# Kernel optimization log

Measured on AMD Instinct MI355X. Metric: run time of the kernel, lower is better.

## Reference

```python
import jax, jax.numpy as jnp
import numpy as np

B, S, DM, H = 4, 2048, 1024, 16
D = DM // H  # head dim = 64

def setup_inputs() -> dict:
    key = jax.random.key(0)
    ks = jax.random.split(key, 7)
    s = 0.02
    return {
        "hidden_states": jax.random.normal(ks[0], (B, S, DM), jnp.float32),
        "attention_mask": jnp.zeros((B, 1, 1, S), jnp.float32),
        "Wq": jax.random.normal(ks[1], (DM, DM), jnp.float32) * s,
        "bq": jnp.zeros((DM,), jnp.float32),
        "Wk": jax.random.normal(ks[2], (DM, DM), jnp.float32) * s,
        "bk": jnp.zeros((DM,), jnp.float32),
        "Wv": jax.random.normal(ks[3], (DM, DM), jnp.float32) * s,
        "bv": jnp.zeros((DM,), jnp.float32),
    }

def _heads(x):
    # [B,S,DM] -> [B,H,S,D]
    return x.reshape(B, S, H, D).transpose(0, 2, 1, 3)

def reference(hidden_states, attention_mask, Wq, bq, Wk, bk, Wv, bv):
    q = _heads(hidden_states @ Wq + bq)
    k = _heads(hidden_states @ Wk + bk)
    v = _heads(hidden_states @ Wv + bv)
    scores = jnp.einsum("bhqd,bhkd->bhqk", q, k) / jnp.sqrt(jnp.float32(D))
    scores = scores + attention_mask
    probs = jax.nn.softmax(scores, axis=-1)  # dropout p=0 -> identity
    ctx = jnp.einsum("bhqk,bhkd->bhqd", probs, v)
    ctx = ctx.transpose(0, 2, 1, 3).reshape(B, S, DM)
    return (ctx, probs)
```

## Files before the change

### kernel.cpp

```cpp
#include <hip/hip_runtime.h>

#define SEQ    2048
#define DMODEL 1024
#define NHEAD  16
#define HDIM   64
#define NBATCH 4
#define LOG2E  1.44269504088896f

typedef __bf16 bf16x8 __attribute__((ext_vector_type(8)));
typedef float  f32x4  __attribute__((ext_vector_type(4)));
typedef unsigned short ushort8_t __attribute__((ext_vector_type(8)));
typedef unsigned short ushort4_t __attribute__((ext_vector_type(4)));

__device__ __forceinline__ unsigned short bfc(float f) {
  union { __bf16 h; unsigned short u; } v;
  v.h = (__bf16)f;
  return v.u;
}

__device__ __forceinline__ float fexp2(float x) {
#if __has_builtin(__builtin_amdgcn_exp2f)
  return __builtin_amdgcn_exp2f(x);
#else
  return exp2f(x);
#endif
}

__device__ __forceinline__ void glds16(const void* g, void* l) {
  __builtin_amdgcn_global_load_lds(
      (const __attribute__((address_space(1))) unsigned int*)g,
      (__attribute__((address_space(3))) unsigned int*)l, 16, 0, 0);
}

__global__ __launch_bounds__(256) void xconv(
    const float* __restrict__ X, unsigned short* __restrict__ Xb)
{
  const size_t i = ((size_t)blockIdx.x * 256 + threadIdx.x) * 8;
  const float4 f0 = *reinterpret_cast<const float4*>(X + i);
  const float4 f1 = *reinterpret_cast<const float4*>(X + i + 4);
  ushort8_t u;
  u[0]=bfc(f0.x); u[1]=bfc(f0.y); u[2]=bfc(f0.z); u[3]=bfc(f0.w);
  u[4]=bfc(f1.x); u[5]=bfc(f1.y); u[6]=bfc(f1.z); u[7]=bfc(f1.w);
  *reinterpret_cast<ushort8_t*>(Xb + i) = u;
}

__global__ __launch_bounds__(256) void wt_kernel(
    const float* __restrict__ W0, const float* __restrict__ W1,
    const float* __restrict__ W2, unsigned short* __restrict__ Wt)
{
  const int k0 = blockIdx.x * 64;
  const int n0 = blockIdx.y * 64;
  const int w  = blockIdx.z;
  const float* W = (w == 0) ? W0 : (w == 1) ? W1 : W2;
  const float scale = (w == 0) ? 0.125f * LOG2E : 1.0f;
  unsigned short* dst = Wt + (size_t)w * DMODEL * DMODEL;

  __shared__ __align__(16) unsigned short T[64][72];
  const int t = threadIdx.x;

  #pragma unroll
  for (int i = 0; i < 4; ++i) {
    const int slot = t + i * 256;
    const int row  = slot >> 4;
    const int c4   = (slot & 15) * 4;
    const float4 f = *reinterpret_cast<const float4*>(W + (size_t)(k0 + row) * DMODEL + n0 + c4);
    ushort4_t u;
    u.x = bfc(f.x * scale); u.y = bfc(f.y * scale);
    u.z = bfc(f.z * scale); u.w = bfc(f.w * scale);
    *reinterpret_cast<ushort4_t*>(&T[row][c4]) = u;
  }
  __syncthreads();
  #pragma unroll
  for (int i = 0; i < 2; ++i) {
    const int slot = t + i * 256;
    const int n  = slot >> 3;
    const int k8 = (slot & 7) * 8;
    ushort8_t v;
    #pragma unroll
    for (int j = 0; j < 8; ++j) v[j] = T[k8 + j][n];
    *reinterpret_cast<ushort8_t*>(dst + (size_t)(n0 + n) * DMODEL + k0 + k8) = v;
  }
}

__global__ __launch_bounds__(256) void qkv_gemm(
    const unsigned short* __restrict__ Xb, const unsigned short* __restrict__ Wt,
    const float* __restrict__ bq, const float* __restrict__ bk, const float* __restrict__ bv,
    unsigned short* __restrict__ Qh, unsigned short* __restrict__ Kh, unsigned short* __restrict__ Vh)
{
  const int m0  = blockIdx.x * 128;
  const int n0g = blockIdx.y * 128;
  const int w   = n0g >> 10;
  const float* bias = (w == 0) ? bq : (w == 1) ? bk : bv;
  unsigned short* dst = (w == 0) ? Qh : (w == 1) ? Kh : Vh;
  const float bscale = (w == 0) ? 0.125f * LOG2E : 1.0f;

  __shared__ __align__(16) unsigned short As[128 * 64];
  __shared__ __align__(16) unsigned short Bs[128 * 64];

  const int t = threadIdx.x;
  const int lane = t & 63;
  const int wid  = t >> 6;
  const int wm = wid >> 1, wn = wid & 1;
  const int lr = lane & 15, lg = lane >> 4;

  const f32x4 fz = {0.f, 0.f, 0.f, 0.f};
  f32x4 acc[4][4];
  #pragma unroll
  for (int i = 0; i < 4; ++i)
    #pragma unroll
    for (int j = 0; j < 4; ++j) acc[i][j] = fz;

  const int srow = t >> 3;
  const int sg   = t & 7;

  for (int k0 = 0; k0 < DMODEL; k0 += 64) {
    #pragma unroll
    for (int i = 0; i < 4; ++i) {
      const int row = i * 32 + srow;
      const int gs  = sg ^ (row & 7);
      glds16(Xb + (size_t)(m0 + row) * DMODEL + k0 + gs * 8,
             (void*)(As + row * 64 + sg * 8));
      glds16(Wt + (size_t)(n0g + row) * DMODEL + k0 + gs * 8,
             (void*)(Bs + row * 64 + sg * 8));
    }
    __syncthreads();

    #pragma unroll
    for (int ks = 0; ks < 2; ++ks) {
      bf16x8 a[4], b[4];
      #pragma unroll
      for (int mi = 0; mi < 4; ++mi) {
        const int row = wm * 64 + mi * 16 + lr;
        a[mi] = *reinterpret_cast<const bf16x8*>(As + row * 64 + ((ks * 4 + lg) ^ (row & 7)) * 8);
      }
      #pragma unroll
      for (int ni = 0; ni < 4; ++ni) {
        const int row = wn * 64 + ni * 16 + lr;
        b[ni] = *reinterpret_cast<const bf16x8*>(Bs + row * 64 + ((ks * 4 + lg) ^ (row & 7)) * 8);
      }
      #pragma unroll
      for (int mi = 0; mi < 4; ++mi)
        #pragma unroll
        for (int ni = 0; ni < 4; ++ni)
          acc[mi][ni] = __builtin_amdgcn_mfma_f32_16x16x32_bf16(a[mi], b[ni], acc[mi][ni], 0, 0, 0);
    }
    __syncthreads();
  }

  #pragma unroll
  for (int mi = 0; mi < 4; ++mi) {
    #pragma unroll
    for (int ni = 0; ni < 4; ++ni) {
      const int n = (n0g & 1023) + wn * 64 + ni * 16 + lr;
      const float bn = bias[n] * bscale;
      const int h = n >> 6, d = n & 63;
      #pragma unroll
      for (int r = 0; r < 4; ++r) {
        const int m = m0 + wm * 64 + mi * 16 + lg * 4 + r;
        const int bb = m >> 11, ss = m & (SEQ - 1);
        dst[(((size_t)(bb * NHEAD + h)) * SEQ + ss) * HDIM + d] = bfc(acc[mi][ni][r] + bn);
      }
    }
  }
}

__global__ __launch_bounds__(256) void vt_kernel(
    const unsigned short* __restrict__ Vh, unsigned short* __restrict__ Vt)
{
  const int s0 = blockIdx.x * 64;
  const int bh = blockIdx.y;
  __shared__ __align__(16) unsigned short T[64][72];
  const int t = threadIdx.x;
  const int row = t >> 3;
  const int c8  = (t & 7) * 8;
  #pragma unroll
  for (int c = 0; c < 2; ++c) {
    const int rr = row + c * 32;
    *reinterpret_cast<ushort8_t*>(&T[rr][c8]) =
      *reinterpret_cast<const ushort8_t*>(Vh + ((size_t)bh * SEQ + s0 + rr) * HDIM + c8);
  }
  __syncthreads();
  #pragma unroll
  for (int i = 0; i < 2; ++i) {
    const int slot = t + i * 256;
    const int d  = slot >> 3;
    const int s8 = (slot & 7) * 8;
    ushort8_t v;
    #pragma unroll
    for (int j = 0; j < 8; ++j) v[j] = T[s8 + j][d];
    *reinterpret_cast<ushort8_t*>(Vt + ((size_t)bh * HDIM + d) * SEQ + s0 + s8) = v;
  }
}

__global__ __launch_bounds__(256) void attn_kernel(
    const unsigned short* __restrict__ Qh, const unsigned short* __restrict__ Kh,
    const unsigned short* __restrict__ Vt, const float* __restrict__ mask,
    float* __restrict__ ctx_out, float* __restrict__ probs_out)
{
  const int bid = blockIdx.x;
  const int L   = (bid & 7) * 256 + (bid >> 3);
  const int qt  = L & 31;
  const int bh  = L >> 5;
  const int h   = bh & (NHEAD - 1);
  const int b   = bh >> 4;

  const int t = threadIdx.x;
  const int lane = t & 63;
  const int wid = t >> 6;
  const int lr = lane & 15, lg = lane >> 4;

  __shared__ __align__(16) unsigned short Qs[64][72];
  __shared__ __align__(16) unsigned short Ps[64][72];
  __shared__ __align__(16) unsigned short Ks[2][64 * 64];
  __shared__ __align__(16) unsigned short Vs[2][64 * 64];

  const size_t qkv_base = (size_t)bh * SEQ * HDIM;
  const size_t vbase    = (size_t)bh * HDIM * SEQ;

  {
    const int srow = t >> 3, sc8 = (t & 7) * 8;
    #pragma unroll
    for (int c = 0; c < 2; ++c) {
      const int rr = srow + c * 32;
      *reinterpret_cast<ushort8_t*>(&Qs[rr][sc8]) =
        *reinterpret_cast<const ushort8_t*>(Qh + qkv_base + (size_t)(qt*64 + rr) * HDIM + sc8);
    }
  }
  __syncthreads();

  bf16x8 qa[2];
  qa[0] = *reinterpret_cast<const bf16x8*>(&Qs[wid*16 + lr][lg*8]);
  qa[1] = *reinterpret_cast<const bf16x8*>(&Qs[wid*16 + lr][32 + lg*8]);

  const int krow = t >> 3;
  const int ksg  = t & 7;

  auto stageK = [&](int buf, int kt) {
    #pragma unroll
    for (int i = 0; i < 2; ++i) {
      const int row = i * 32 + krow;
      glds16(Kh + qkv_base + (size_t)(kt*64 + row) * HDIM + ((ksg ^ (row & 7)) * 8),
             (void*)(&Ks[buf][row * 64 + ksg * 8]));
    }
  };
  auto stageV = [&](int buf, int kt) {
    #pragma unroll
    for (int i = 0; i < 2; ++i) {
      const int row = i * 32 + krow;
      glds16(Vt + vbase + (size_t)row * SEQ + kt*64 + ((ksg ^ (row & 7)) * 8),
             (void*)(&Vs[buf][row * 64 + ksg * 8]));
    }
  };

  const float* maskb = mask + b * SEQ;
  const f32x4 fz = {0.f, 0.f, 0.f, 0.f};

  float l_lane = 0.f;

  stageK(0, 0);
  asm volatile("s_waitcnt vmcnt(0)" ::: "memory");
  __builtin_amdgcn_sched_barrier(0);
  __builtin_amdgcn_s_barrier();

  for (int kt = 0; kt < SEQ / 64; ++kt) {
    const int cur = kt & 1;
    if (kt < SEQ / 64 - 1) stageK(cur ^ 1, kt + 1);
    __builtin_amdgcn_sched_barrier(0);

    f32x4 s[4];
    #pragma unroll
    for (int ni = 0; ni < 4; ++ni) s[ni] = fz;
    __builtin_amdgcn_s_setprio(1);
    #pragma unroll
    for (int kd = 0; kd < 2; ++kd) {
      #pragma unroll
      for (int ni = 0; ni < 4; ++ni) {
        const int row = ni*16 + lr;
        const bf16x8 kb = *reinterpret_cast<const bf16x8*>(
            &Ks[cur][row * 64 + ((kd*4 + lg) ^ (lr & 7)) * 8]);
        s[ni] = __builtin_amdgcn_mfma_f32_16x16x32_bf16(kb, qa[kd], s[ni], 0, 0, 0);
      }
    }
    __builtin_amdgcn_s_setprio(0);
    #pragma unroll
    for (int ni = 0; ni < 4; ++ni) {
      const float4 mv = *reinterpret_cast<const float4*>(&maskb[kt*64 + ni*16 + lg*4]);
      l_lane += fexp2(s[ni][0] + mv.x * LOG2E);
      l_lane += fexp2(s[ni][1] + mv.y * LOG2E);
      l_lane += fexp2(s[ni][2] + mv.z * LOG2E);
      l_lane += fexp2(s[ni][3] + mv.w * LOG2E);
    }
    __builtin_amdgcn_sched_barrier(0);
    asm volatile("s_waitcnt vmcnt(0)" ::: "memory");
    __builtin_amdgcn_sched_barrier(0);
    __builtin_amdgcn_s_barrier();
  }

  float l = l_lane;
  l += __shfl_xor(l, 16);
  l += __shfl_xor(l, 32);
  const float inv_l = 1.0f / l;

  f32x4 cacc[4];
  #pragma unroll
  for (int nd = 0; nd < 4; ++nd) cacc[nd] = fz;

  const size_t pbase = ((size_t)bh * SEQ + qt*64) * SEQ;

  stageK(0, 0); stageV(0, 0);
  asm volatile("s_waitcnt vmcnt(0)" ::: "memory");
  __builtin_amdgcn_sched_barrier(0);
  __builtin_amdgcn_s_barrier();

  for (int kt = 0; kt < SEQ / 64; ++kt) {
    const int cur = kt & 1;
    const bool pre = (kt < SEQ / 64 - 1);
    if (pre) { stageK(cur ^ 1, kt + 1); stageV(cur ^ 1, kt + 1); }
    __builtin_amdgcn_sched_barrier(0);

    f32x4 s[4];
    #pragma unroll
    for (int ni = 0; ni < 4; ++ni) s[ni] = fz;
    __builtin_amdgcn_s_setprio(1);
    #pragma unroll
    for (int kd = 0; kd < 2; ++kd) {
      #pragma unroll
      for (int ni = 0; ni < 4; ++ni) {
        const int row = ni*16 + lr;
        const bf16x8 kb = *reinterpret_cast<const bf16x8*>(
            &Ks[cur][row * 64 + ((kd*4 + lg) ^ (lr & 7)) * 8]);
        s[ni] = __builtin_amdgcn_mfma_f32_16x16x32_bf16(kb, qa[kd], s[ni], 0, 0, 0);
      }
    }
    __builtin_amdgcn_s_setprio(0);

    float* prow = probs_out + pbase + (size_t)(wid*16 + lr) * SEQ + kt*64;
    unsigned short* psrow = &Ps[wid*16 + lr][0];
    #pragma unroll
    for (int ni = 0; ni < 4; ++ni) {
      const float4 mv = *reinterpret_cast<const float4*>(&maskb[kt*64 + ni*16 + lg*4]);
      f32x4 p;
      p[0] = fexp2(s[ni][0] + mv.x * LOG2E) * inv_l;
      p[1] = fexp2(s[ni][1] + mv.y * LOG2E) * inv_l;
      p[2] = fexp2(s[ni][2] + mv.z * LOG2E) * inv_l;
      p[3] = fexp2(s[ni][3] + mv.w * LOG2E) * inv_l;
      __builtin_nontemporal_store(p, reinterpret_cast<f32x4*>(prow + ni*16 + lg*4));
      ushort4_t pu;
      pu[0] = bfc(p[0]); pu[1] = bfc(p[1]); pu[2] = bfc(p[2]); pu[3] = bfc(p[3]);
      const int g = (2*ni + (lg >> 1)) ^ (lr & 7);
      *reinterpret_cast<ushort4_t*>(psrow + g*8 + (lg & 1)*4) = pu;
    }

    __builtin_amdgcn_s_setprio(1);
    #pragma unroll
    for (int ks = 0; ks < 2; ++ks) {
      const bf16x8 pb = *reinterpret_cast<const bf16x8*>(
          psrow + ((4*ks + lg) ^ (lr & 7)) * 8);
      #pragma unroll
      for (int nd = 0; nd < 4; ++nd) {
        const int row = nd*16 + lr;
        const bf16x8 vb = *reinterpret_cast<const bf16x8*>(
            &Vs[cur][row * 64 + ((ks*4 + lg) ^ (lr & 7)) * 8]);
        cacc[nd] = __builtin_amdgcn_mfma_f32_16x16x32_bf16(vb, pb, cacc[nd], 0, 0, 0);
      }
    }
    __builtin_amdgcn_s_setprio(0);

    __builtin_amdgcn_sched_barrier(0);
    if (pre) {
      asm volatile("s_waitcnt vmcnt(4)" ::: "memory");
    }
    __builtin_amdgcn_sched_barrier(0);
    __builtin_amdgcn_s_barrier();
  }

  const int q = qt*64 + wid*16 + lr;
  float* crow = ctx_out + ((size_t)(b * SEQ + q)) * DMODEL + h * HDIM;
  #pragma unroll
  for (int nd = 0; nd < 4; ++nd) {
    __builtin_nontemporal_store(cacc[nd], reinterpret_cast<f32x4*>(crow + nd*16 + lg*4));
  }
}

extern "C" void kernel_launch(void* const* d_in, const int* in_sizes, int n_in,
                              void* d_out, int out_size, void* d_ws, size_t ws_size,
                              hipStream_t stream)
{
  const float* X    = (const float*)d_in[0];
  const float* mask = (const float*)d_in[1];
  const float* Wq   = (const float*)d_in[2];
  const float* bq   = (const float*)d_in[3];
  const float* Wk   = (const float*)d_in[4];
  const float* bk   = (const float*)d_in[5];
  const float* Wv   = (const float*)d_in[6];
  const float* bv   = (const float*)d_in[7];

  float* ctx   = (float*)d_out;
  float* probs = ctx + (size_t)NBATCH * SEQ * DMODEL;

  unsigned short* Wt = (unsigned short*)d_ws;
  unsigned short* Xb = Wt + (size_t)3 * DMODEL * DMODEL;
  unsigned short* Qh = Xb + (size_t)NBATCH * SEQ * DMODEL;
  unsigned short* Kh = Qh + (size_t)NBATCH * NHEAD * SEQ * HDIM;
  unsigned short* Vh = Kh + (size_t)NBATCH * NHEAD * SEQ * HDIM;
  unsigned short* Vt = Vh + (size_t)NBATCH * NHEAD * SEQ * HDIM;

  xconv<<<dim3(4096), 256, 0, stream>>>(X, Xb);
  wt_kernel<<<dim3(16, 16, 3), 256, 0, stream>>>(Wq, Wk, Wv, Wt);
  qkv_gemm<<<dim3(64, 24), 256, 0, stream>>>(Xb, Wt, bq, bk, bv, Qh, Kh, Vh);
  vt_kernel<<<dim3(32, NBATCH * NHEAD), 256, 0, stream>>>(Vh, Vt);
  attn_kernel<<<dim3(2048), 256, 0, stream>>>(Qh, Kh, Vt, mask, ctx, probs);
}
```

Before: 420.2 us.

## Double query tile per block to 128 rows and stage pre-scaled mask in LDS

Each attention block now handles 128 query rows (two 16-row groups per wave), so every K/V tile loaded into LDS is reused by twice as many MFMAs and the grid is halved. The mask is pre-multiplied by log2(e) in a new small kernel and staged into LDS alongside K via global_load_lds, replacing per-lane global mask loads. The Q and P shared buffers are merged to save LDS. The cost is more accumulator registers per thread, which may lower occupancy, and an extra kernel launch.

```diff
diff --git a/kernel.cpp b/kernel.cpp
--- a/kernel.cpp
+++ b/kernel.cpp
@@ -30,6 +30,11 @@
   __builtin_amdgcn_global_load_lds(
       (const __attribute__((address_space(1))) unsigned int*)g,
       (__attribute__((address_space(3))) unsigned int*)l, 16, 0, 0);
+}
+__device__ __forceinline__ void glds4(const void* g, void* l) {
+  __builtin_amdgcn_global_load_lds(
+      (const __attribute__((address_space(1))) unsigned int*)g,
+      (__attribute__((address_space(3))) unsigned int*)l, 4, 0, 0);
 }
 
 __global__ __launch_bounds__(256) void xconv(
@@ -42,6 +47,13 @@
   u[0]=bfc(f0.x); u[1]=bfc(f0.y); u[2]=bfc(f0.z); u[3]=bfc(f0.w);
   u[4]=bfc(f1.x); u[5]=bfc(f1.y); u[6]=bfc(f1.z); u[7]=bfc(f1.w);
   *reinterpret_cast<ushort8_t*>(Xb + i) = u;
+}
+
+__global__ __launch_bounds__(256) void mscale(
+    const float* __restrict__ mask, float* __restrict__ m2)
+{
+  const int i = blockIdx.x * 256 + threadIdx.x;
+  m2[i] = mask[i] * LOG2E;
 }
 
 __global__ __launch_bounds__(256) void wt_kernel(
@@ -194,13 +206,13 @@
 
 __global__ __launch_bounds__(256) void attn_kernel(
     const unsigned short* __restrict__ Qh, const unsigned short* __restrict__ Kh,
-    const unsigned short* __restrict__ Vt, const float* __restrict__ mask,
+    const unsigned short* __restrict__ Vt, const float* __restrict__ m2,
     float* __restrict__ ctx_out, float* __restrict__ probs_out)
 {
   const int bid = blockIdx.x;
-  const int L   = (bid & 7) * 256 + (bid >> 3);
-  const int qt  = L & 31;
-  const int bh  = L >> 5;
+  const int L   = (bid & 7) * 128 + (bid >> 3);
+  const int qt  = L & 15;
+  const int bh  = L >> 4;
   const int h   = bh & (NHEAD - 1);
   const int b   = bh >> 4;
 
@@ -209,10 +221,10 @@
   const int wid = t >> 6;
   const int lr = lane & 15, lg = lane >> 4;
 
-  __shared__ __align__(16) unsigned short Qs[64][72];
-  __shared__ __align__(16) unsigned short Ps[64][72];
+  __shared__ __align__(16) unsigned short QP[128 * 72];
   __shared__ __align__(16) unsigned short Ks[2][64 * 64];
   __shared__ __align__(16) unsigned short Vs[2][64 * 64];
+  __shared__ __align__(16) float Ms[2][64];
 
   const size_t qkv_base = (size_t)bh * SEQ * HDIM;
   const size_t vbase    = (size_t)bh * HDIM * SEQ;
@@ -220,20 +232,26 @@
   {
     const int srow = t >> 3, sc8 = (t & 7) * 8;
     #pragma unroll
-    for (int c = 0; c < 2; ++c) {
+    for (int c = 0; c < 4; ++c) {
       const int rr = srow + c * 32;
-      *reinterpret_cast<ushort8_t*>(&Qs[rr][sc8]) =
-        *reinterpret_cast<const ushort8_t*>(Qh + qkv_base + (size_t)(qt*64 + rr) * HDIM + sc8);
+      *reinterpret_cast<ushort8_t*>(&QP[rr * 72 + sc8]) =
+        *reinterpret_cast<const ushort8_t*>(Qh + qkv_base + (size_t)(qt*128 + rr) * HDIM + sc8);
     }
   }
   __syncthreads();
 
-  bf16x8 qa[2];
-  qa[0] = *reinterpret_cast<const bf16x8*>(&Qs[wid*16 + lr][lg*8]);
-  qa[1] = *reinterpret_cast<const bf16x8*>(&Qs[wid*16 + lr][32 + lg*8]);
+  bf16x8 qa[2][2];
+  #pragma unroll
+  for (int qg = 0; qg < 2; ++qg)
+    #pragma unroll
+    for (int kd = 0; kd < 2; ++kd)
+      qa[qg][kd] = *reinterpret_cast<const bf16x8*>(
+          &QP[(wid*32 + qg*16 + lr) * 72 + kd*32 + lg*8]);
+  __syncthreads();
 
   const int krow = t >> 3;
   const int ksg  = t & 7;
+  const float* m2b = m2 + b * SEQ;
 
   auto stageK = [&](int buf, int kt) {
     #pragma unroll
@@ -242,6 +260,7 @@
       glds16(Kh + qkv_base + (size_t)(kt*64 + row) * HDIM + ((ksg ^ (row & 7)) * 8),
              (void*)(&Ks[buf][row * 64 + ksg * 8]));
     }
+    if (wid == 0) glds4(m2b + kt*64 + lane, (void*)(&Ms[buf][0]));
   };
   auto stageV = [&](int buf, int kt) {
     #pragma unroll
@@ -252,10 +271,8 @@
     }
   };
 
-  const float* maskb = mask + b * SEQ;
   const f32x4 fz = {0.f, 0.f, 0.f, 0.f};
-
-  float l_lane = 0.f;
+  float l_lane[2] = {0.f, 0.f};
 
   stageK(0, 0);
   asm volatile("s_waitcnt vmcnt(0)" ::: "memory");
@@ -267,9 +284,11 @@
     if (kt < SEQ / 64 - 1) stageK(cur ^ 1, kt + 1);
     __builtin_amdgcn_sched_barrier(0);
 
-    f32x4 s[4];
-    #pragma unroll
-    for (int ni = 0; ni < 4; ++ni) s[ni] = fz;
+    f32x4 s[2][4];
+    #pragma unroll
+    for (int qg = 0; qg < 2; ++qg)
+      #pragma unroll
+      for (int ni = 0; ni < 4; ++ni) s[qg][ni] = fz;
     __builtin_amdgcn_s_setprio(1);
     #pragma unroll
     for (int kd = 0; kd < 2; ++kd) {
@@ -278,17 +297,22 @@
         const int row = ni*16 + lr;
         const bf16x8 kb = *reinterpret_cast<const bf16x8*>(
             &Ks[cur][row * 64 + ((kd*4 + lg) ^ (lr & 7)) * 8]);
-        s[ni] = __builtin_amdgcn_mfma_f32_16x16x32_bf16(kb, qa[kd], s[ni], 0, 0, 0);
+        #pragma unroll
+        for (int qg = 0; qg < 2; ++qg)
+          s[qg][ni] = __builtin_amdgcn_mfma_f32_16x16x32_bf16(kb, qa[qg][kd], s[qg][ni], 0, 0, 0);
       }
     }
     __builtin_amdgcn_s_setprio(0);
     #pragma unroll
     for (int ni = 0; ni < 4; ++ni) {
-      const float4 mv = *reinterpret_cast<const float4*>(&maskb[kt*64 + ni*16 + lg*4]);
-      l_lane += fexp2(s[ni][0] + mv.x * LOG2E);
-      l_lane += fexp2(s[ni][1] + mv.y * LOG2E);
-      l_lane += fexp2(s[ni][2] + mv.z * LOG2E);
-      l_lane += fexp2(s[ni][3] + mv.w * LOG2E);
+      const f32x4 mv = *reinterpret_cast<const f32x4*>(&Ms[cur][ni*16 + lg*4]);
+      #pragma unroll
+      for (int qg = 0; qg < 2; ++qg) {
+        l_lane[qg] += fexp2(s[qg][ni][0] + mv[0]);
+        l_lane[qg] += fexp2(s[qg][ni][1] + mv[1]);
+        l_lane[qg] += fexp2(s[qg][ni][2] + mv[2]);
+        l_lane[qg] += fexp2(s[qg][ni][3] + mv[3]);
+      }
     }
     __builtin_amdgcn_sched_barrier(0);
     asm volatile("s_waitcnt vmcnt(0)" ::: "memory");
@@ -296,16 +320,22 @@
     __builtin_amdgcn_s_barrier();
   }
 
-  float l = l_lane;
-  l += __shfl_xor(l, 16);
-  l += __shfl_xor(l, 32);
-  const float inv_l = 1.0f / l;
-
-  f32x4 cacc[4];
-  #pragma unroll
-  for (int nd = 0; nd < 4; ++nd) cacc[nd] = fz;
-
-  const size_t pbase = ((size_t)bh * SEQ + qt*64) * SEQ;
+  float inv_l[2];
+  #pragma unroll
+  for (int qg = 0; qg < 2; ++qg) {
+    float l = l_lane[qg];
+    l += __shfl_xor(l, 16);
+    l += __shfl_xor(l, 32);
+    inv_l[qg] = 1.0f / l;
+  }
+
+  f32x4 cacc[4][2];
+  #pragma unroll
+  for (int nd = 0; nd < 4; ++nd)
+    #pragma unroll
+    for (int qg = 0; qg < 2; ++qg) cacc[nd][qg] = fz;
+
+  const size_t pbase = ((size_t)bh * SEQ + qt*128) * SEQ;
 
   stageK(0, 0); stageV(0, 0);
   asm volatile("s_waitcnt vmcnt(0)" ::: "memory");
@@ -318,9 +348,11 @@
     if (pre) { stageK(cur ^ 1, kt + 1); stageV(cur ^ 1, kt + 1); }
     __builtin_amdgcn_sched_barrier(0);
 
-    f32x4 s[4];
-    #pragma unroll
-    for (int ni = 0; ni < 4; ++ni) s[ni] = fz;
+    f32x4 s[2][4];
+    #pragma unroll
+    for (int qg = 0; qg < 2; ++qg)
+      #pragma unroll
+      for (int ni = 0; ni < 4; ++ni) s[qg][ni] = fz;
     __builtin_amdgcn_s_setprio(1);
     #pragma unroll
     for (int kd = 0; kd < 2; ++kd) {
@@ -329,56 +361,68 @@
         const int row = ni*16 + lr;
         const bf16x8 kb = *reinterpret_cast<const bf16x8*>(
             &Ks[cur][row * 64 + ((kd*4 + lg) ^ (lr & 7)) * 8]);
-        s[ni] = __builtin_amdgcn_mfma_f32_16x16x32_bf16(kb, qa[kd], s[ni], 0, 0, 0);
+        #pragma unroll
+        for (int qg = 0; qg < 2; ++qg)
+          s[qg][ni] = __builtin_amdgcn_mfma_f32_16x16x32_bf16(kb, qa[qg][kd], s[qg][ni], 0, 0, 0);
       }
     }
     __builtin_amdgcn_s_setprio(0);
 
-    float* prow = probs_out + pbase + (size_t)(wid*16 + lr) * SEQ + kt*64;
-    unsigned short* psrow = &Ps[wid*16 + lr][0];
-    #pragma unroll
-    for (int ni = 0; ni < 4; ++ni) {
-      const float4 mv = *reinterpret_cast<const float4*>(&maskb[kt*64 + ni*16 + lg*4]);
-      f32x4 p;
-      p[0] = fexp2(s[ni][0] + mv.x * LOG2E) * inv_l;
-      p[1] = fexp2(s[ni][1] + mv.y * LOG2E) * inv_l;
-      p[2] = fexp2(s[ni][2] + mv.z * LOG2E) * inv_l;
-      p[3] = fexp2(s[ni][3] + mv.w * LOG2E) * inv_l;
-      __builtin_nontemporal_store(p, reinterpret_cast<f32x4*>(prow + ni*16 + lg*4));
-      ushort4_t pu;
-      pu[0] = bfc(p[0]); pu[1] = bfc(p[1]); pu[2] = bfc(p[2]); pu[3] = bfc(p[3]);
-      const int g = (2*ni + (lg >> 1)) ^ (lr & 7);
-      *reinterpret_cast<ushort4_t*>(psrow + g*8 + (lg & 1)*4) = pu;
+    #pragma unroll
+    for (int qg = 0; qg < 2; ++qg) {
+      float* prow = probs_out + pbase + (size_t)(wid*32 + qg*16 + lr) * SEQ + kt*64;
+      unsigned short* psrow = &QP[(wid*32 + qg*16 + lr) * 72];
+      #pragma unroll
+      for (int ni = 0; ni < 4; ++ni) {
+        const f32x4 mv = *reinterpret_cast<const f32x4*>(&Ms[cur][ni*16 + lg*4]);
+        f32x4 p;
+        p[0] = fexp2(s[qg][ni][0] + mv[0]) * inv_l[qg];
+        p[1] = fexp2(s[qg][ni][1] + mv[1]) * inv_l[qg];
+        p[2] = fexp2(s[qg][ni][2] + mv[2]) * inv_l[qg];
+        p[3] = fexp2(s[qg][ni][3] + mv[3]) * inv_l[qg];
+        __builtin_nontemporal_store(p, reinterpret_cast<f32x4*>(prow + ni*16 + lg*4));
+        ushort4_t pu;
+        pu[0] = bfc(p[0]); pu[1] = bfc(p[1]); pu[2] = bfc(p[2]); pu[3] = bfc(p[3]);
+        const int g = (2*ni + (lg >> 1)) ^ (lr & 7);
+        *reinterpret_cast<ushort4_t*>(psrow + g*8 + (lg & 1)*4) = pu;
+      }
     }
 
     __builtin_amdgcn_s_setprio(1);
     #pragma unroll
     for (int ks = 0; ks < 2; ++ks) {
-      const bf16x8 pb = *reinterpret_cast<const bf16x8*>(
-          psrow + ((4*ks + lg) ^ (lr & 7)) * 8);
+      bf16x8 pb[2];
+      #pragma unroll
+      for (int qg = 0; qg < 2; ++qg)
+        pb[qg] = *reinterpret_cast<const bf16x8*>(
+            &QP[(wid*32 + qg*16 + lr) * 72 + ((4*ks + lg) ^ (lr & 7)) * 8]);
       #pragma unroll
       for (int nd = 0; nd < 4; ++nd) {
         const int row = nd*16 + lr;
         const bf16x8 vb = *reinterpret_cast<const bf16x8*>(
             &Vs[cur][row * 64 + ((ks*4 + lg) ^ (lr & 7)) * 8]);
-        cacc[nd] = __builtin_amdgcn_mfma_f32_16x16x32_bf16(vb, pb, cacc[nd], 0, 0, 0);
+        #pragma unroll
+        for (int qg = 0; qg < 2; ++qg)
+          cacc[nd][qg] = __builtin_amdgcn_mfma_f32_16x16x32_bf16(vb, pb[qg], cacc[nd][qg], 0, 0, 0);
       }
     }
     __builtin_amdgcn_s_setprio(0);
 
     __builtin_amdgcn_sched_barrier(0);
     if (pre) {
-      asm volatile("s_waitcnt vmcnt(4)" ::: "memory");
+      asm volatile("s_waitcnt vmcnt(8)" ::: "memory");
     }
     __builtin_amdgcn_sched_barrier(0);
     __builtin_amdgcn_s_barrier();
   }
 
-  const int q = qt*64 + wid*16 + lr;
-  float* crow = ctx_out + ((size_t)(b * SEQ + q)) * DMODEL + h * HDIM;
-  #pragma unroll
-  for (int nd = 0; nd < 4; ++nd) {
-    __builtin_nontemporal_store(cacc[nd], reinterpret_cast<f32x4*>(crow + nd*16 + lg*4));
+  #pragma unroll
+  for (int qg = 0; qg < 2; ++qg) {
+    const int q = qt*128 + wid*32 + qg*16 + lr;
+    float* crow = ctx_out + ((size_t)(b * SEQ + q)) * DMODEL + h * HDIM;
+    #pragma unroll
+    for (int nd = 0; nd < 4; ++nd)
+      __builtin_nontemporal_store(cacc[nd][qg], reinterpret_cast<f32x4*>(crow + nd*16 + lg*4));
   }
 }
 
@@ -404,10 +448,12 @@
   unsigned short* Kh = Qh + (size_t)NBATCH * NHEAD * SEQ * HDIM;
   unsigned short* Vh = Kh + (size_t)NBATCH * NHEAD * SEQ * HDIM;
   unsigned short* Vt = Vh + (size_t)NBATCH * NHEAD * SEQ * HDIM;
+  float* m2 = (float*)(Vt + (size_t)NBATCH * NHEAD * SEQ * HDIM);
 
   xconv<<<dim3(4096), 256, 0, stream>>>(X, Xb);
+  mscale<<<dim3(NBATCH * SEQ / 256), 256, 0, stream>>>(mask, m2);
   wt_kernel<<<dim3(16, 16, 3), 256, 0, stream>>>(Wq, Wk, Wv, Wt);
   qkv_gemm<<<dim3(64, 24), 256, 0, stream>>>(Xb, Wt, bq, bk, bv, Qh, Kh, Vh);
   vt_kernel<<<dim3(32, NBATCH * NHEAD), 256, 0, stream>>>(Vh, Vt);
-  attn_kernel<<<dim3(2048), 256, 0, stream>>>(Qh, Kh, Vt, mask, ctx, probs);
-}
+  attn_kernel<<<dim3(1024), 256, 0, stream>>>(Qh, Kh, Vt, m2, ctx, probs);
+}
```

Result: slower. 467.5 us (+11.2%).

## Split softmax row-sum pass into separate kernel and stage premultiplied mask in LDS

Applied to the files above, without the earlier changes.

The single attention kernel, which ran a row-sum pass and then a probs/context pass, is split into two kernels. lsum_kernel computes the inverse row sums into workspace, and attn2_kernel reads them and does only the output pass. Both kernels load the mask once into shared memory already multiplied by log2e, and attn2 reuses the Q buffer for P to keep LDS usage down. The split is meant to give each kernel fewer registers and less LDS, allowing higher occupancy and overlap, at the cost of an extra launch, a small global round trip and reading Q/K twice across kernels.

```diff
diff --git a/kernel.cpp b/kernel.cpp
--- a/kernel.cpp
+++ b/kernel.cpp
@@ -192,10 +192,116 @@
   }
 }
 
-__global__ __launch_bounds__(256) void attn_kernel(
+__global__ __launch_bounds__(256) void lsum_kernel(
+    const unsigned short* __restrict__ Qh, const unsigned short* __restrict__ Kh,
+    const float* __restrict__ mask, float* __restrict__ linv)
+{
+  const int bid = blockIdx.x;
+  const int L   = (bid & 7) * 256 + (bid >> 3);
+  const int qt  = L & 31;
+  const int bh  = L >> 5;
+  const int b   = bh >> 4;
+
+  const int t = threadIdx.x;
+  const int lane = t & 63;
+  const int wid = t >> 6;
+  const int lr = lane & 15, lg = lane >> 4;
+
+  __shared__ __align__(16) unsigned short Qs[64][72];
+  __shared__ __align__(16) unsigned short Ks[2][64 * 64];
+  __shared__ __align__(16) float Msk[SEQ];
+
+  const size_t qkv_base = (size_t)bh * SEQ * HDIM;
+
+  {
+    const int srow = t >> 3, sc8 = (t & 7) * 8;
+    #pragma unroll
+    for (int c = 0; c < 2; ++c) {
+      const int rr = srow + c * 32;
+      *reinterpret_cast<ushort8_t*>(&Qs[rr][sc8]) =
+        *reinterpret_cast<const ushort8_t*>(Qh + qkv_base + (size_t)(qt*64 + rr) * HDIM + sc8);
+    }
+    const float* maskb = mask + b * SEQ;
+    #pragma unroll
+    for (int i = 0; i < 2; ++i) {
+      const int slot = t + i * 256;
+      const float4 mv = *reinterpret_cast<const float4*>(maskb + slot * 4);
+      f32x4 m4; m4[0]=mv.x*LOG2E; m4[1]=mv.y*LOG2E; m4[2]=mv.z*LOG2E; m4[3]=mv.w*LOG2E;
+      *reinterpret_cast<f32x4*>(&Msk[slot * 4]) = m4;
+    }
+  }
+  __syncthreads();
+
+  bf16x8 qa[2];
+  qa[0] = *reinterpret_cast<const bf16x8*>(&Qs[wid*16 + lr][lg*8]);
+  qa[1] = *reinterpret_cast<const bf16x8*>(&Qs[wid*16 + lr][32 + lg*8]);
+
+  const int krow = t >> 3;
+  const int ksg  = t & 7;
+
+  auto stageK = [&](int buf, int kt) {
+    #pragma unroll
+    for (int i = 0; i < 2; ++i) {
+      const int row = i * 32 + krow;
+      glds16(Kh + qkv_base + (size_t)(kt*64 + row) * HDIM + ((ksg ^ (row & 7)) * 8),
+             (void*)(&Ks[buf][row * 64 + ksg * 8]));
+    }
+  };
+
+  const f32x4 fz = {0.f, 0.f, 0.f, 0.f};
+  float l0 = 0.f, l1 = 0.f;
+
+  stageK(0, 0);
+  asm volatile("s_waitcnt vmcnt(0)" ::: "memory");
+  __builtin_amdgcn_sched_barrier(0);
+  __builtin_amdgcn_s_barrier();
+
+  for (int kt = 0; kt < SEQ / 64; ++kt) {
+    const int cur = kt & 1;
+    if (kt < SEQ / 64 - 1) stageK(cur ^ 1, kt + 1);
+    __builtin_amdgcn_sched_barrier(0);
+
+    f32x4 s[4];
+    #pragma unroll
+    for (int ni = 0; ni < 4; ++ni) s[ni] = fz;
+    __builtin_amdgcn_s_setprio(1);
+    #pragma unroll
+    for (int kd = 0; kd < 2; ++kd) {
+      #pragma unroll
+      for (int ni = 0; ni < 4; ++ni) {
+        const int row = ni*16 + lr;
+        const bf16x8 kb = *reinterpret_cast<const bf16x8*>(
+            &Ks[cur][row * 64 + ((kd*4 + lg) ^ (lr & 7)) * 8]);
+        s[ni] = __builtin_amdgcn_mfma_f32_16x16x32_bf16(kb, qa[kd], s[ni], 0, 0, 0);
+      }
+    }
+    __builtin_amdgcn_s_setprio(0);
+    #pragma unroll
+    for (int ni = 0; ni < 4; ++ni) {
+      const f32x4 mv = *reinterpret_cast<const f32x4*>(&Msk[kt*64 + ni*16 + lg*4]);
+      l0 += fexp2(s[ni][0] + mv[0]);
+      l1 += fexp2(s[ni][1] + mv[1]);
+      l0 += fexp2(s[ni][2] + mv[2]);
+      l1 += fexp2(s[ni][3] + mv[3]);
+    }
+    __builtin_amdgcn_sched_barrier(0);
+    asm volatile("s_waitcnt vmcnt(0)" ::: "memory");
+    __builtin_amdgcn_sched_barrier(0);
+    __builtin_amdgcn_s_barrier();
+  }
+
+  float l = l0 + l1;
+  l += __shfl_xor(l, 16);
+  l += __shfl_xor(l, 32);
+  if (lg == 0)
+    linv[(size_t)bh * SEQ + qt*64 + wid*16 + lr] = 1.0f / l;
+}
+
+__global__ __launch_bounds__(256) void attn2_kernel(
     const unsigned short* __restrict__ Qh, const unsigned short* __restrict__ Kh,
     const unsigned short* __restrict__ Vt, const float* __restrict__ mask,
-    float* __restrict__ ctx_out, float* __restrict__ probs_out)
+    const float* __restrict__ linv, float* __restrict__ ctx_out,
+    float* __restrict__ probs_out)
 {
   const int bid = blockIdx.x;
   const int L   = (bid & 7) * 256 + (bid >> 3);
@@ -209,10 +315,10 @@
   const int wid = t >> 6;
   const int lr = lane & 15, lg = lane >> 4;
 
-  __shared__ __align__(16) unsigned short Qs[64][72];
-  __shared__ __align__(16) unsigned short Ps[64][72];
+  __shared__ __align__(16) unsigned short QP[64 * 72];
   __shared__ __align__(16) unsigned short Ks[2][64 * 64];
   __shared__ __align__(16) unsigned short Vs[2][64 * 64];
+  __shared__ __align__(16) float Msk[SEQ];
 
   const size_t qkv_base = (size_t)bh * SEQ * HDIM;
   const size_t vbase    = (size_t)bh * HDIM * SEQ;
@@ -222,15 +328,25 @@
     #pragma unroll
     for (int c = 0; c < 2; ++c) {
       const int rr = srow + c * 32;
-      *reinterpret_cast<ushort8_t*>(&Qs[rr][sc8]) =
+      *reinterpret_cast<ushort8_t*>(&QP[rr * 72 + sc8]) =
         *reinterpret_cast<const ushort8_t*>(Qh + qkv_base + (size_t)(qt*64 + rr) * HDIM + sc8);
     }
+    const float* maskb = mask + b * SEQ;
+    #pragma unroll
+    for (int i = 0; i < 2; ++i) {
+      const int slot = t + i * 256;
+      const float4 mv = *reinterpret_cast<const float4*>(maskb + slot * 4);
+      f32x4 m4; m4[0]=mv.x*LOG2E; m4[1]=mv.y*LOG2E; m4[2]=mv.z*LOG2E; m4[3]=mv.w*LOG2E;
+      *reinterpret_cast<f32x4*>(&Msk[slot * 4]) = m4;
+    }
   }
   __syncthreads();
 
   bf16x8 qa[2];
-  qa[0] = *reinterpret_cast<const bf16x8*>(&Qs[wid*16 + lr][lg*8]);
-  qa[1] = *reinterpret_cast<const bf16x8*>(&Qs[wid*16 + lr][32 + lg*8]);
+  qa[0] = *reinterpret_cast<const bf16x8*>(&QP[(wid*16 + lr) * 72 + lg*8]);
+  qa[1] = *reinterpret_cast<const bf16x8*>(&QP[(wid*16 + lr) * 72 + 32 + lg*8]);
+  const float inv_l = linv[(size_t)bh * SEQ + qt*64 + wid*16 + lr];
+  __syncthreads();
 
   const int krow = t >> 3;
   const int ksg  = t & 7;
@@ -252,19 +368,22 @@
     }
   };
 
-  const float* maskb = mask + b * SEQ;
   const f32x4 fz = {0.f, 0.f, 0.f, 0.f};
-
-  float l_lane = 0.f;
-
-  stageK(0, 0);
+  f32x4 cacc[4];
+  #pragma unroll
+  for (int nd = 0; nd < 4; ++nd) cacc[nd] = fz;
+
+  const size_t pbase = ((size_t)bh * SEQ + qt*64) * SEQ;
+
+  stageK(0, 0); stageV(0, 0);
   asm volatile("s_waitcnt vmcnt(0)" ::: "memory");
   __builtin_amdgcn_sched_barrier(0);
   __builtin_amdgcn_s_barrier();
 
   for (int kt = 0; kt < SEQ / 64; ++kt) {
     const int cur = kt & 1;
-    if (kt < SEQ / 64 - 1) stageK(cur ^ 1, kt + 1);
+    const bool pre = (kt < SEQ / 64 - 1);
+    if (pre) { stageK(cur ^ 1, kt + 1); stageV(cur ^ 1, kt + 1); }
     __builtin_amdgcn_sched_barrier(0);
 
     f32x4 s[4];
@@ -282,68 +401,17 @@
       }
     }
     __builtin_amdgcn_s_setprio(0);
+
+    float* prow = probs_out + pbase + (size_t)(wid*16 + lr) * SEQ + kt*64;
+    unsigned short* psrow = &QP[(wid*16 + lr) * 72];
     #pragma unroll
     for (int ni = 0; ni < 4; ++ni) {
-      const float4 mv = *reinterpret_cast<const float4*>(&maskb[kt*64 + ni*16 + lg*4]);
-      l_lane += fexp2(s[ni][0] + mv.x * LOG2E);
-      l_lane += fexp2(s[ni][1] + mv.y * LOG2E);
-      l_lane += fexp2(s[ni][2] + mv.z * LOG2E);
-      l_lane += fexp2(s[ni][3] + mv.w * LOG2E);
-    }
-    __builtin_amdgcn_sched_barrier(0);
-    asm volatile("s_waitcnt vmcnt(0)" ::: "memory");
-    __builtin_amdgcn_sched_barrier(0);
-    __builtin_amdgcn_s_barrier();
-  }
-
-  float l = l_lane;
-  l += __shfl_xor(l, 16);
-  l += __shfl_xor(l, 32);
-  const float inv_l = 1.0f / l;
-
-  f32x4 cacc[4];
-  #pragma unroll
-  for (int nd = 0; nd < 4; ++nd) cacc[nd] = fz;
-
-  const size_t pbase = ((size_t)bh * SEQ + qt*64) * SEQ;
-
-  stageK(0, 0); stageV(0, 0);
-  asm volatile("s_waitcnt vmcnt(0)" ::: "memory");
-  __builtin_amdgcn_sched_barrier(0);
-  __builtin_amdgcn_s_barrier();
-
-  for (int kt = 0; kt < SEQ / 64; ++kt) {
-    const int cur = kt & 1;
-    const bool pre = (kt < SEQ / 64 - 1);
-    if (pre) { stageK(cur ^ 1, kt + 1); stageV(cur ^ 1, kt + 1); }
-    __builtin_amdgcn_sched_barrier(0);
-
-    f32x4 s[4];
-    #pragma unroll
-    for (int ni = 0; ni < 4; ++ni) s[ni] = fz;
-    __builtin_amdgcn_s_setprio(1);
-    #pragma unroll
-    for (int kd = 0; kd < 2; ++kd) {
-      #pragma unroll
-      for (int ni = 0; ni < 4; ++ni) {
-        const int row = ni*16 + lr;
-        const bf16x8 kb = *reinterpret_cast<const bf16x8*>(
-            &Ks[cur][row * 64 + ((kd*4 + lg) ^ (lr & 7)) * 8]);
-        s[ni] = __builtin_amdgcn_mfma_f32_16x16x32_bf16(kb, qa[kd], s[ni], 0, 0, 0);
-      }
-    }
-    __builtin_amdgcn_s_setprio(0);
-
-    float* prow = probs_out + pbase + (size_t)(wid*16 + lr) * SEQ + kt*64;
-    unsigned short* psrow = &Ps[wid*16 + lr][0];
-    #pragma unroll
-    for (int ni = 0; ni < 4; ++ni) {
-      const float4 mv = *reinterpret_cast<const float4*>(&maskb[kt*64 + ni*16 + lg*4]);
+      const f32x4 mv = *reinterpret_cast<const f32x4*>(&Msk[kt*64 + ni*16 + lg*4]);
       f32x4 p;
-      p[0] = fexp2(s[ni][0] + mv.x * LOG2E) * inv_l;
-      p[1] = fexp2(s[ni][1] + mv.y * LOG2E) * inv_l;
-      p[2] = fexp2(s[ni][2] + mv.z * LOG2E) * inv_l;
-      p[3] = fexp2(s[ni][3] + mv.w * LOG2E) * inv_l;
+      p[0] = fexp2(s[ni][0] + mv[0]) * inv_l;
+      p[1] = fexp2(s[ni][1] + mv[1]) * inv_l;
+      p[2] = fexp2(s[ni][2] + mv[2]) * inv_l;
+      p[3] = fexp2(s[ni][3] + mv[3]) * inv_l;
       __builtin_nontemporal_store(p, reinterpret_cast<f32x4*>(prow + ni*16 + lg*4));
       ushort4_t pu;
       pu[0] = bfc(p[0]); pu[1] = bfc(p[1]); pu[2] = bfc(p[2]); pu[3] = bfc(p[3]);
@@ -377,9 +445,8 @@
   const int q = qt*64 + wid*16 + lr;
   float* crow = ctx_out + ((size_t)(b * SEQ + q)) * DMODEL + h * HDIM;
   #pragma unroll
-  for (int nd = 0; nd < 4; ++nd) {
+  for (int nd = 0; nd < 4; ++nd)
     __builtin_nontemporal_store(cacc[nd], reinterpret_cast<f32x4*>(crow + nd*16 + lg*4));
-  }
 }
 
 extern "C" void kernel_launch(void* const* d_in, const int* in_sizes, int n_in,
@@ -404,10 +471,12 @@
   unsigned short* Kh = Qh + (size_t)NBATCH * NHEAD * SEQ * HDIM;
   unsigned short* Vh = Kh + (size_t)NBATCH * NHEAD * SEQ * HDIM;
   unsigned short* Vt = Vh + (size_t)NBATCH * NHEAD * SEQ * HDIM;
+  float* linv = (float*)(Vt + (size_t)NBATCH * NHEAD * SEQ * HDIM);
 
   xconv<<<dim3(4096), 256, 0, stream>>>(X, Xb);
   wt_kernel<<<dim3(16, 16, 3), 256, 0, stream>>>(Wq, Wk, Wv, Wt);
   qkv_gemm<<<dim3(64, 24), 256, 0, stream>>>(Xb, Wt, bq, bk, bv, Qh, Kh, Vh);
   vt_kernel<<<dim3(32, NBATCH * NHEAD), 256, 0, stream>>>(Vh, Vt);
-  attn_kernel<<<dim3(2048), 256, 0, stream>>>(Qh, Kh, Vt, mask, ctx, probs);
-}
+  lsum_kernel<<<dim3(2048), 256, 0, stream>>>(Qh, Kh, mask, linv);
+  attn2_kernel<<<dim3(2048), 256, 0, stream>>>(Qh, Kh, Vt, mask, linv, ctx, probs);
+}
```

New measurement: 464.5 us. 1.11x slower.
